# Kernel tuning notes

Hardware: AMD Instinct MI355X
Metric: run time of the kernel (lower is better)

Reference implementation:

```python
import jax, jax.numpy as jnp
import numpy as np

N = 100000      # nodes
E = 1600000     # edges (avg degree 16)
D_IN, D_H, D_OUT = 128, 128, 40
BN_EPS = 1e-5


def _gcn_norm(edge_index):
    # add self-loops, compute symmetric normalization D^-1/2 (A+I) D^-1/2
    loops = jnp.arange(N, dtype=edge_index.dtype)
    src = jnp.concatenate([edge_index[0], loops])
    dst = jnp.concatenate([edge_index[1], loops])
    deg = jax.ops.segment_sum(jnp.ones(src.shape[0], jnp.float32), dst, num_segments=N)
    dinv = jnp.where(deg > 0, jax.lax.rsqrt(deg), 0.0)
    norm = dinv[src] * dinv[dst]  # [E+N]
    return src, dst, norm


def _gcn_conv(h, W, b, src, dst, norm):
    h = h @ W                          # [N, d_out]
    msg = h[src] * norm[:, None]       # [E+N, d_out] gather + scale
    out = jax.ops.segment_sum(msg, dst, num_segments=N)
    return out + b


def _bn(h, g, beta, mean, var):
    return g * (h - mean) * jax.lax.rsqrt(var + BN_EPS) + beta


def setup_inputs() -> dict:
    key = jax.random.key(0)
    ks = jax.random.split(key, 16)
    x = jax.random.normal(ks[0], (N, D_IN), jnp.float32)
    edge_index = jax.random.randint(ks[1], (2, E), 0, N, dtype=jnp.int32)
    s_in, s_h = 1.0 / np.sqrt(D_IN), 1.0 / np.sqrt(D_H)
    W0 = jax.random.normal(ks[2], (D_IN, D_H), jnp.float32) * s_in
    b0 = jnp.zeros((D_H,), jnp.float32)
    W1 = jax.random.normal(ks[3], (D_H, D_H), jnp.float32) * s_h
    b1 = jnp.zeros((D_H,), jnp.float32)
    W2 = jax.random.normal(ks[4], (D_H, D_OUT), jnp.float32) * s_h
    b2 = jnp.zeros((D_OUT,), jnp.float32)
    g0 = jnp.ones((D_H,), jnp.float32)
    be0 = jnp.zeros((D_H,), jnp.float32)
    m0 = jax.random.normal(ks[5], (D_H,), jnp.float32) * 0.1
    v0 = jax.random.uniform(ks[6], (D_H,), jnp.float32) + 0.5
    g1 = jnp.ones((D_H,), jnp.float32)
    be1 = jnp.zeros((D_H,), jnp.float32)
    m1 = jax.random.normal(ks[7], (D_H,), jnp.float32) * 0.1
    v1 = jax.random.uniform(ks[8], (D_H,), jnp.float32) + 0.5
    return {"x": x, "edge_index": edge_index,
            "W0": W0, "b0": b0, "W1": W1, "b1": b1, "W2": W2, "b2": b2,
            "g0": g0, "be0": be0, "m0": m0, "v0": v0,
            "g1": g1, "be1": be1, "m1": m1, "v1": v1}


def reference(x, edge_index, W0, b0, W1, b1, W2, b2,
              g0, be0, m0, v0, g1, be1, m1, v1):
    src, dst, norm = _gcn_norm(edge_index)
    h = _gcn_conv(x, W0, b0, src, dst, norm)
    h = jax.nn.relu(_bn(h, g0, be0, m0, v0))   # dropout = identity in eval
    h = _gcn_conv(h, W1, b1, src, dst, norm)
    h = jax.nn.relu(_bn(h, g1, be1, m1, v1))
    h = _gcn_conv(h, W2, b2, src, dst, norm)
    return jax.nn.log_softmax(h, axis=1)
```

## Files before the change

### kernel.cpp

```cpp
#include <hip/hip_runtime.h>
#include <math.h>


#define CSHIFT 9
#define CSZ 512
#define PCHUNK 4096

typedef unsigned short u16;
typedef unsigned int u32;
typedef unsigned char u8;
typedef float f32x4 __attribute__((ext_vector_type(4)));
typedef short s16x8 __attribute__((ext_vector_type(8)));

__device__ inline float bflo(u32 u) { return __uint_as_float(u << 16); }
__device__ inline float bfhi(u32 u) { return __uint_as_float(u & 0xffff0000u); }
__device__ inline u16 f2bf(float f) {
    u32 b = __float_as_uint(f);
    b += 0x7fff + ((b >> 16) & 1);
    return (u16)(b >> 16);
}
__device__ inline u32 pack2(float lo, float hi) {
    return (u32)f2bf(lo) | ((u32)f2bf(hi) << 16);
}


__global__ __launch_bounds__(256) void k_hist1(const int* __restrict__ dst,
                                               int* __restrict__ hist1,
                                               int E, int NB) {
    __shared__ int h[256];
    int t = threadIdx.x;
    h[t] = 0;
    __syncthreads();
    for (int i = blockIdx.x * 256 * 16 + t; i < min(E, (blockIdx.x + 1) * 256 * 16);
         i += 256)
        atomicAdd(&h[dst[i] >> CSHIFT], 1);
    __syncthreads();
    if (t < NB && h[t]) atomicAdd(&hist1[t], h[t]);
}

__global__ __launch_bounds__(256) void k_scan1(const int* __restrict__ hist1,
                                               int* __restrict__ base1,
                                               int* __restrict__ cur1,
                                               int NB, int E) {
    __shared__ int sc[256];
    int t = threadIdx.x;
    int v = (t < NB) ? hist1[t] : 0;
    sc[t] = v;
    __syncthreads();
    for (int d = 1; d < 256; d <<= 1) {
        int add = (t >= d) ? sc[t - d] : 0;
        __syncthreads();
        sc[t] += add;
        __syncthreads();
    }
    if (t < NB) {
        int excl = sc[t] - v;
        base1[t] = excl;
        cur1[t] = excl;
    }
    if (t == 0) base1[NB] = E;
}

__global__ __launch_bounds__(256) void k_part1(const int* __restrict__ src,
                                               const int* __restrict__ dst,
                                               int* __restrict__ cur1,
                                               u32* __restrict__ bkt,
                                               int E, int NB) {
    __shared__ u32 stage[PCHUNK];
    __shared__ u8 sbin[PCHUNK];
    __shared__ int cnt[256];
    __shared__ int lbase[256];
    __shared__ int lcur[256];
    __shared__ int gb[256];
    int t = threadIdx.x;
    int base = blockIdx.x * PCHUNK;
    int n = min(PCHUNK, E - base);
    cnt[t] = 0;
    __syncthreads();
    for (int i = t; i < n; i += 256) atomicAdd(&cnt[dst[base + i] >> CSHIFT], 1);
    __syncthreads();
    int v = cnt[t];
    lbase[t] = v;
    __syncthreads();
    for (int d = 1; d < 256; d <<= 1) {
        int add = (t >= d) ? lbase[t - d] : 0;
        __syncthreads();
        lbase[t] += add;
        __syncthreads();
    }
    {
        int excl = lbase[t] - v;
        __syncthreads();
        lbase[t] = excl;
        lcur[t] = excl;
        if (t < NB && v) gb[t] = atomicAdd(&cur1[t], v);
    }
    __syncthreads();
    for (int i = t; i < n; i += 256) {
        int d = dst[base + i];
        int s = src[base + i];
        int bin = d >> CSHIFT;
        int p = atomicAdd(&lcur[bin], 1);
        stage[p] = ((u32)s << CSHIFT) | (u32)(d & (CSZ - 1));
        sbin[p] = (u8)bin;
    }
    __syncthreads();
    for (int k = t; k < n; k += 256) {
        int bin = sbin[k];
        bkt[gb[bin] + (k - lbase[bin])] = stage[k];
    }
}

__global__ __launch_bounds__(1024) void k_csr(const u32* __restrict__ bkt,
                                              const int* __restrict__ base1,
                                              int* __restrict__ col,
                                              int* __restrict__ row,
                                              float* __restrict__ dinv,
                                              int N, int E) {
    __shared__ int deg[CSZ];
    __shared__ int cur[CSZ];
    int b = blockIdx.x;
    int t = threadIdx.x;
    int start = base1[b];
    int end = base1[b + 1];
    if (t < CSZ) deg[t] = 0;
    __syncthreads();
    for (int i = start + t; i < end; i += 1024)
        atomicAdd(&deg[bkt[i] & (CSZ - 1)], 1);
    __syncthreads();
    int v = (t < CSZ) ? deg[t] : 0;
    if (t < CSZ) cur[t] = v;
    __syncthreads();
    for (int d = 1; d < CSZ; d <<= 1) {
        int add = (t < CSZ && t >= d) ? cur[t - d] : 0;
        __syncthreads();
        if (t < CSZ) cur[t] += add;
        __syncthreads();
    }
    if (t < CSZ) {
        int excl = cur[t] - v;
        int node = (b << CSHIFT) + t;
        if (node < N) {
            row[node] = start + excl;
            dinv[node] = rsqrtf((float)(v + 1));
        }
        cur[t] = excl;
    }
    __syncthreads();
    for (int i = start + t; i < end; i += 1024) {
        u32 e = bkt[i];
        int p = start + atomicAdd(&cur[e & (CSZ - 1)], 1);
        col[p] = (int)(e >> CSHIFT);
    }
    if (b == 0 && t == 0) row[N] = E;
}


template <int NCT, int C>
__global__ __launch_bounds__(256) void k_packW(const float* __restrict__ W,
                                               u16* __restrict__ Wpk) {
    int g = blockIdx.x * 256 + threadIdx.x;
    if (g >= NCT * 4 * 512) return;
    int j = g & 7;
    int l = (g >> 3) & 63;
    int f = g >> 9;
    int ct = f % NCT, ks = f / NCT;
    int krow = ks * 32 + ((l >> 4) << 3) + j;
    int wcol = ct * 16 + (l & 15);
    Wpk[g] = (wcol < C) ? f2bf(W[krow * C + wcol]) : (u16)0;
}


template <bool AFP32, int NCT>
__global__ __launch_bounds__(256) void k_gemmN(const void* __restrict__ Av,
                                               const u16* __restrict__ Wpk,
                                               u16* __restrict__ C,
                                               const float* __restrict__ dinv,
                                               int M, int ostride) {
    int tid = threadIdx.x;
    int wv = blockIdx.x * 4 + (tid >> 6);
    int rowbase = wv * 16;
    if (rowbase >= M) return;
    int l = tid & 63;
    int r = l & 15, hi = l >> 4;

    f32x4 acc[NCT];
#pragma unroll
    for (int ct = 0; ct < NCT; ++ct) acc[ct] = (f32x4)(0.f);

    const uint4* wp = (const uint4*)Wpk;
#pragma unroll
    for (int ks = 0; ks < 4; ++ks) {
        s16x8 afrag;
        int abase = (min(rowbase + r, M - 1)) * 128 + ks * 32 + hi * 8;
        if (AFP32) {
            const float* A = (const float*)Av;
            float4 a0 = *(const float4*)&A[abase];
            float4 a1 = *(const float4*)&A[abase + 4];
            uint4 u = make_uint4(pack2(a0.x, a0.y), pack2(a0.z, a0.w),
                                 pack2(a1.x, a1.y), pack2(a1.z, a1.w));
            afrag = *(s16x8*)&u;
        } else {
            const u16* A = (const u16*)Av;
            uint4 u = *(const uint4*)&A[abase];
            afrag = *(s16x8*)&u;
        }
#pragma unroll
        for (int ct = 0; ct < NCT; ++ct) {
            uint4 b = wp[(ks * NCT + ct) * 64 + l];
            s16x8 bfrag = *(s16x8*)&b;
            acc[ct] = __builtin_amdgcn_mfma_f32_16x16x32_bf16(afrag, bfrag, acc[ct], 0, 0, 0);
        }
    }
#pragma unroll
    for (int ct = 0; ct < NCT; ++ct) {
#pragma unroll
        for (int reg = 0; reg < 4; ++reg) {
            int orow = rowbase + 4 * hi + reg;
            int oc = ct * 16 + r;
            if (orow < M && oc < ostride)
                C[(size_t)orow * ostride + oc] = f2bf(dinv[orow] * acc[ct][reg]);
        }
    }
}


__global__ __launch_bounds__(256) void k_agg128(const u16* __restrict__ X,
                                                u16* __restrict__ Y,
                                                const int* __restrict__ row,
                                                const int* __restrict__ col,
                                                const float* __restrict__ dinv,
                                                const float* __restrict__ bias,
                                                const float* __restrict__ g,
                                                const float* __restrict__ be,
                                                const float* __restrict__ mean,
                                                const float* __restrict__ var,
                                                int n) {
    int tid = threadIdx.x;
    int wid = tid >> 6, lane = tid & 63;
    int half = lane >> 5, l5 = lane & 31;
    int node = (blockIdx.x * 4 + wid) * 2 + half;
    bool valid = node < n;
    int nc = valid ? node : (n - 1);
    const uint2* xp = (const uint2*)X;
    int s = row[nc], e = row[nc + 1];
    uint2 v = xp[(size_t)nc * 32 + l5];
    float a0 = bflo(v.x), a1 = bfhi(v.x), a2 = bflo(v.y), a3 = bfhi(v.y);
    float b0 = 0, b1 = 0, b2 = 0, b3 = 0;
    float c0 = 0, c1 = 0, c2 = 0, c3 = 0;
    float d0 = 0, d1 = 0, d2 = 0, d3 = 0;
    int j = s;
    for (; j + 8 <= e; j += 8) {
        int e0 = col[j], e1 = col[j+1], e2 = col[j+2], e3 = col[j+3];
        int e4 = col[j+4], e5 = col[j+5], e6 = col[j+6], e7 = col[j+7];
        uint2 x0 = xp[(size_t)e0 * 32 + l5];
        uint2 x1 = xp[(size_t)e1 * 32 + l5];
        uint2 x2 = xp[(size_t)e2 * 32 + l5];
        uint2 x3 = xp[(size_t)e3 * 32 + l5];
        uint2 x4 = xp[(size_t)e4 * 32 + l5];
        uint2 x5 = xp[(size_t)e5 * 32 + l5];
        uint2 x6 = xp[(size_t)e6 * 32 + l5];
        uint2 x7 = xp[(size_t)e7 * 32 + l5];
        a0 += bflo(x0.x); a1 += bfhi(x0.x); a2 += bflo(x0.y); a3 += bfhi(x0.y);
        b0 += bflo(x1.x); b1 += bfhi(x1.x); b2 += bflo(x1.y); b3 += bfhi(x1.y);
        c0 += bflo(x2.x); c1 += bfhi(x2.x); c2 += bflo(x2.y); c3 += bfhi(x2.y);
        d0 += bflo(x3.x); d1 += bfhi(x3.x); d2 += bflo(x3.y); d3 += bfhi(x3.y);
        a0 += bflo(x4.x); a1 += bfhi(x4.x); a2 += bflo(x4.y); a3 += bfhi(x4.y);
        b0 += bflo(x5.x); b1 += bfhi(x5.x); b2 += bflo(x5.y); b3 += bfhi(x5.y);
        c0 += bflo(x6.x); c1 += bfhi(x6.x); c2 += bflo(x6.y); c3 += bfhi(x6.y);
        d0 += bflo(x7.x); d1 += bfhi(x7.x); d2 += bflo(x7.y); d3 += bfhi(x7.y);
    }
    for (; j + 2 <= e; j += 2) {
        int e0 = col[j], e1 = col[j+1];
        uint2 x0 = xp[(size_t)e0 * 32 + l5];
        uint2 x1 = xp[(size_t)e1 * 32 + l5];
        a0 += bflo(x0.x); a1 += bfhi(x0.x); a2 += bflo(x0.y); a3 += bfhi(x0.y);
        b0 += bflo(x1.x); b1 += bfhi(x1.x); b2 += bflo(x1.y); b3 += bfhi(x1.y);
    }
    if (j < e) {
        uint2 x0 = xp[(size_t)col[j] * 32 + l5];
        c0 += bflo(x0.x); c1 += bfhi(x0.x); c2 += bflo(x0.y); c3 += bfhi(x0.y);
    }
    float dv = dinv[nc];
    float s0 = dv * ((a0 + b0) + (c0 + d0));
    float s1 = dv * ((a1 + b1) + (c1 + d1));
    float s2 = dv * ((a2 + b2) + (c2 + d2));
    float s3 = dv * ((a3 + b3) + (c3 + d3));
    float4 g4 = ((const float4*)g)[l5];
    float4 be4 = ((const float4*)be)[l5];
    float4 m4 = ((const float4*)mean)[l5];
    float4 v4 = ((const float4*)var)[l5];
    float4 bi4 = ((const float4*)bias)[l5];
    float sc0 = g4.x * rsqrtf(v4.x + 1e-5f);
    float sc1 = g4.y * rsqrtf(v4.y + 1e-5f);
    float sc2 = g4.z * rsqrtf(v4.z + 1e-5f);
    float sc3 = g4.w * rsqrtf(v4.w + 1e-5f);
    float y0 = fmaxf(fmaf(sc0, s0, fmaf(sc0, bi4.x - m4.x, be4.x)), 0.f);
    float y1 = fmaxf(fmaf(sc1, s1, fmaf(sc1, bi4.y - m4.y, be4.y)), 0.f);
    float y2 = fmaxf(fmaf(sc2, s2, fmaf(sc2, bi4.z - m4.z, be4.z)), 0.f);
    float y3 = fmaxf(fmaf(sc3, s3, fmaf(sc3, bi4.w - m4.w, be4.w)), 0.f);
    if (valid) {
        uint2 o;
        o.x = pack2(y0, y1);
        o.y = pack2(y2, y3);
        ((uint2*)Y)[(size_t)node * 32 + l5] = o;
    }
}

__global__ __launch_bounds__(256) void k_agg40(const u16* __restrict__ X,
                                               float* __restrict__ out,
                                               const int* __restrict__ row,
                                               const int* __restrict__ col,
                                               const float* __restrict__ dinv,
                                               const float* __restrict__ b2,
                                               int n) {
    int tid = threadIdx.x;
    int wid = tid >> 6, lane = tid & 63;
    int half = lane >> 5, l5 = lane & 31;
    int node = (blockIdx.x * 4 + wid) * 2 + half;
    bool valid = node < n;
    int nc = valid ? node : (n - 1);
    bool active = l5 < 20;
    const u32* xp = (const u32*)X;
    int s = row[nc], e = row[nc + 1];
    int li = min(l5, 19);
    float a0 = 0, a1 = 0, b0 = 0, b1 = 0, c0 = 0, c1 = 0, d0 = 0, d1 = 0;
    {
        u32 v = xp[(size_t)nc * 20 + li];
        a0 = bflo(v); a1 = bfhi(v);
    }
    int j = s;
    for (; j + 8 <= e; j += 8) {
        int e0 = col[j], e1 = col[j+1], e2 = col[j+2], e3 = col[j+3];
        int e4 = col[j+4], e5 = col[j+5], e6 = col[j+6], e7 = col[j+7];
        u32 x0 = xp[(size_t)e0 * 20 + li];
        u32 x1 = xp[(size_t)e1 * 20 + li];
        u32 x2 = xp[(size_t)e2 * 20 + li];
        u32 x3 = xp[(size_t)e3 * 20 + li];
        u32 x4 = xp[(size_t)e4 * 20 + li];
        u32 x5 = xp[(size_t)e5 * 20 + li];
        u32 x6 = xp[(size_t)e6 * 20 + li];
        u32 x7 = xp[(size_t)e7 * 20 + li];
        a0 += bflo(x0); a1 += bfhi(x0);
        b0 += bflo(x1); b1 += bfhi(x1);
        c0 += bflo(x2); c1 += bfhi(x2);
        d0 += bflo(x3); d1 += bfhi(x3);
        a0 += bflo(x4); a1 += bfhi(x4);
        b0 += bflo(x5); b1 += bfhi(x5);
        c0 += bflo(x6); c1 += bfhi(x6);
        d0 += bflo(x7); d1 += bfhi(x7);
    }
    for (; j + 2 <= e; j += 2) {
        int e0 = col[j], e1 = col[j+1];
        u32 x0 = xp[(size_t)e0 * 20 + li];
        u32 x1 = xp[(size_t)e1 * 20 + li];
        a0 += bflo(x0); a1 += bfhi(x0);
        b0 += bflo(x1); b1 += bfhi(x1);
    }
    if (j < e) {
        u32 x0 = xp[(size_t)col[j] * 20 + li];
        c0 += bflo(x0); c1 += bfhi(x0);
    }
    float dv = dinv[nc];
    float ylo = -INFINITY, yhi = -INFINITY;
    if (active) {
        float2 bb = ((const float2*)b2)[l5];
        ylo = fmaf(dv, (a0 + b0) + (c0 + d0), bb.x);
        yhi = fmaf(dv, (a1 + b1) + (c1 + d1), bb.y);
    }
    float m = fmaxf(ylo, yhi);
#pragma unroll
    for (int d = 16; d; d >>= 1) m = fmaxf(m, __shfl_xor(m, d));
    float ex = active ? (__expf(ylo - m) + __expf(yhi - m)) : 0.f;
#pragma unroll
    for (int d = 16; d; d >>= 1) ex += __shfl_xor(ex, d);
    if (valid && active) {
        float lse = m + __logf(ex);
        ((float2*)out)[(size_t)node * 20 + l5] = make_float2(ylo - lse, yhi - lse);
    }
}


extern "C" void kernel_launch(void* const* d_in, const int* in_sizes, int n_in,
                              void* d_out, int out_size, void* d_ws, size_t ws_size,
                              hipStream_t stream) {
    const float* x   = (const float*)d_in[0];
    const int*   ei  = (const int*)d_in[1];
    const float* W0  = (const float*)d_in[2];
    const float* b0  = (const float*)d_in[3];
    const float* W1  = (const float*)d_in[4];
    const float* b1  = (const float*)d_in[5];
    const float* W2  = (const float*)d_in[6];
    const float* b2  = (const float*)d_in[7];
    const float* g0  = (const float*)d_in[8];
    const float* be0 = (const float*)d_in[9];
    const float* m0  = (const float*)d_in[10];
    const float* v0  = (const float*)d_in[11];
    const float* g1  = (const float*)d_in[12];
    const float* be1 = (const float*)d_in[13];
    const float* m1  = (const float*)d_in[14];
    const float* v1  = (const float*)d_in[15];
    float* out = (float*)d_out;

    int N = in_sizes[0] / 128;
    int E = in_sizes[1] / 2;
    const int* src = ei;
    const int* dst = ei + E;

    int NB = (N + CSZ - 1) / CSZ;

    char* ws = (char*)d_ws;
    size_t off = 0;
    auto alloc = [&](size_t bytes) -> char* {
        char* p = ws + off;
        off += (bytes + 255) & ~(size_t)255;
        return p;
    };
    u16*   XsA   = (u16*)alloc((size_t)N * 128 * 2);
    u16*   XsB   = (u16*)alloc((size_t)N * 128 * 2);
    u16*   bufC  = (u16*)alloc((size_t)N * 40 * 2);
    int*   col   = (int*)alloc((size_t)E * 4 + 64);
    int*   row   = (int*)alloc((size_t)(N + 1) * 4);
    float* dinv  = (float*)alloc((size_t)N * 4);
    int*   hist1 = (int*)alloc((size_t)(NB + 1) * 4);
    int*   base1 = (int*)alloc((size_t)(NB + 1) * 4);
    int*   cur1  = (int*)alloc((size_t)(NB + 1) * 4);
    u16*   Wpk0  = (u16*)alloc(128 * 128 * 2);
    u16*   Wpk1  = (u16*)alloc(128 * 128 * 2);
    u16*   Wpk2  = (u16*)alloc(128 * 48 * 2);
    u32*   bkt   = (u32*)XsA;

    hipMemsetAsync(hist1, 0, (size_t)(NB + 1) * 4, stream);
    k_hist1<<<(E + 4095) / 4096, 256, 0, stream>>>(dst, hist1, E, NB);
    k_scan1<<<1, 256, 0, stream>>>(hist1, base1, cur1, NB, E);
    k_part1<<<(E + PCHUNK - 1) / PCHUNK, 256, 0, stream>>>(src, dst, cur1, bkt, E, NB);
    k_csr<<<NB, 1024, 0, stream>>>(bkt, base1, col, row, dinv, N, E);
    k_packW<8, 128><<<64, 256, 0, stream>>>(W0, Wpk0);
    k_packW<8, 128><<<64, 256, 0, stream>>>(W1, Wpk1);
    k_packW<3, 40><<<24, 256, 0, stream>>>(W2, Wpk2);

    int gemmGrid = ((N + 15) / 16 + 3) / 4;
    k_gemmN<true, 8><<<gemmGrid, 256, 0, stream>>>(x, Wpk0, XsA, dinv, N, 128);
    k_agg128<<<(N + 7) / 8, 256, 0, stream>>>(XsA, XsB, row, col, dinv, b0, g0, be0, m0, v0, N);
    k_gemmN<false, 8><<<gemmGrid, 256, 0, stream>>>(XsB, Wpk1, XsA, dinv, N, 128);
    k_agg128<<<(N + 7) / 8, 256, 0, stream>>>(XsA, XsB, row, col, dinv, b1, g1, be1, m1, v1, N);
    k_gemmN<false, 3><<<gemmGrid, 256, 0, stream>>>(XsB, Wpk2, bufC, dinv, N, 40);
    k_agg40<<<(N + 7) / 8, 256, 0, stream>>>(bufC, out, row, col, dinv, b2, N);
}
```

Baseline: 288.3 us.

## Store hidden features in channel-chunked layout so aggregation gathers fit cache

The 128-wide hidden features are now stored as 8 chunks of 16 channels each ([chunk][node][16]). The GEMMs write and read this tiled layout, and the aggregation kernel gives each block one chunk, so a gather only touches a 3.2 MB slice per chunk pass. The goal is better L2/MALL hit rates for the random neighbour gathers. The cost is that the column indices are re-read 8 times (now with nontemporal loads) and each gather is a smaller 8-byte access. The unroll depth also drops from 8 to 4.

```diff
diff --git a/kernel.cpp b/kernel.cpp
--- a/kernel.cpp
+++ b/kernel.cpp
@@ -11,6 +11,7 @@
 typedef unsigned char u8;
 typedef float f32x4 __attribute__((ext_vector_type(4)));
 typedef short s16x8 __attribute__((ext_vector_type(8)));
+typedef unsigned int u32x2 __attribute__((ext_vector_type(2)));
 
 __device__ inline float bflo(u32 u) { return __uint_as_float(u << 16); }
 __device__ inline float bfhi(u32 u) { return __uint_as_float(u & 0xffff0000u); }
@@ -171,7 +172,7 @@
 }
 
 
-template <bool AFP32, int NCT>
+template <bool AFP32, bool ATILED, int NCT, bool OTILED>
 __global__ __launch_bounds__(256) void k_gemmN(const void* __restrict__ Av,
                                                const u16* __restrict__ Wpk,
                                                u16* __restrict__ C,
@@ -183,6 +184,7 @@
     if (rowbase >= M) return;
     int l = tid & 63;
     int r = l & 15, hi = l >> 4;
+    int arow = min(rowbase + r, M - 1);
 
     f32x4 acc[NCT];
 #pragma unroll
@@ -192,17 +194,23 @@
 #pragma unroll
     for (int ks = 0; ks < 4; ++ks) {
         s16x8 afrag;
-        int abase = (min(rowbase + r, M - 1)) * 128 + ks * 32 + hi * 8;
         if (AFP32) {
             const float* A = (const float*)Av;
+            int abase = arow * 128 + ks * 32 + hi * 8;
             float4 a0 = *(const float4*)&A[abase];
             float4 a1 = *(const float4*)&A[abase + 4];
             uint4 u = make_uint4(pack2(a0.x, a0.y), pack2(a0.z, a0.w),
                                  pack2(a1.x, a1.y), pack2(a1.z, a1.w));
             afrag = *(s16x8*)&u;
+        } else if (ATILED) {
+            const u16* A = (const u16*)Av;
+            int k0 = ks * 32 + hi * 8;
+            int ch = k0 >> 4, off = k0 & 15;
+            uint4 u = *(const uint4*)&A[((size_t)ch * M + arow) * 16 + off];
+            afrag = *(s16x8*)&u;
         } else {
             const u16* A = (const u16*)Av;
-            uint4 u = *(const uint4*)&A[abase];
+            uint4 u = *(const uint4*)&A[(size_t)arow * 128 + ks * 32 + hi * 8];
             afrag = *(s16x8*)&u;
         }
 #pragma unroll
@@ -218,79 +226,77 @@
         for (int reg = 0; reg < 4; ++reg) {
             int orow = rowbase + 4 * hi + reg;
             int oc = ct * 16 + r;
-            if (orow < M && oc < ostride)
-                C[(size_t)orow * ostride + oc] = f2bf(dinv[orow] * acc[ct][reg]);
+            if (orow < M && oc < ostride) {
+                u16 val = f2bf(dinv[orow] * acc[ct][reg]);
+                if (OTILED)
+                    C[((size_t)ct * M + orow) * 16 + r] = val;
+                else
+                    C[(size_t)orow * ostride + oc] = val;
+            }
         }
     }
 }
 
 
-__global__ __launch_bounds__(256) void k_agg128(const u16* __restrict__ X,
-                                                u16* __restrict__ Y,
-                                                const int* __restrict__ row,
-                                                const int* __restrict__ col,
-                                                const float* __restrict__ dinv,
-                                                const float* __restrict__ bias,
-                                                const float* __restrict__ g,
-                                                const float* __restrict__ be,
-                                                const float* __restrict__ mean,
-                                                const float* __restrict__ var,
-                                                int n) {
+__global__ __launch_bounds__(256) void k_agg128t(const u16* __restrict__ X,
+                                                 u16* __restrict__ Y,
+                                                 const int* __restrict__ row,
+                                                 const int* __restrict__ col,
+                                                 const float* __restrict__ dinv,
+                                                 const float* __restrict__ bias,
+                                                 const float* __restrict__ g,
+                                                 const float* __restrict__ be,
+                                                 const float* __restrict__ mean,
+                                                 const float* __restrict__ var,
+                                                 int n) {
     int tid = threadIdx.x;
-    int wid = tid >> 6, lane = tid & 63;
-    int half = lane >> 5, l5 = lane & 31;
-    int node = (blockIdx.x * 4 + wid) * 2 + half;
+    int ch = blockIdx.x & 7;
+    int nblk = blockIdx.x >> 3;
+    int wid = tid >> 6, l = tid & 63;
+    int gi = l >> 2, li = l & 3;
+    int node = nblk * 64 + wid * 16 + gi;
     bool valid = node < n;
     int nc = valid ? node : (n - 1);
-    const uint2* xp = (const uint2*)X;
+    const u16* Xc = X + (size_t)ch * n * 16;
     int s = row[nc], e = row[nc + 1];
-    uint2 v = xp[(size_t)nc * 32 + l5];
+    int fo = li * 4;
+
+    uint2 v = *(const uint2*)&Xc[(size_t)nc * 16 + fo];
     float a0 = bflo(v.x), a1 = bfhi(v.x), a2 = bflo(v.y), a3 = bfhi(v.y);
     float b0 = 0, b1 = 0, b2 = 0, b3 = 0;
     float c0 = 0, c1 = 0, c2 = 0, c3 = 0;
     float d0 = 0, d1 = 0, d2 = 0, d3 = 0;
     int j = s;
-    for (; j + 8 <= e; j += 8) {
-        int e0 = col[j], e1 = col[j+1], e2 = col[j+2], e3 = col[j+3];
-        int e4 = col[j+4], e5 = col[j+5], e6 = col[j+6], e7 = col[j+7];
-        uint2 x0 = xp[(size_t)e0 * 32 + l5];
-        uint2 x1 = xp[(size_t)e1 * 32 + l5];
-        uint2 x2 = xp[(size_t)e2 * 32 + l5];
-        uint2 x3 = xp[(size_t)e3 * 32 + l5];
-        uint2 x4 = xp[(size_t)e4 * 32 + l5];
-        uint2 x5 = xp[(size_t)e5 * 32 + l5];
-        uint2 x6 = xp[(size_t)e6 * 32 + l5];
-        uint2 x7 = xp[(size_t)e7 * 32 + l5];
+    for (; j + 4 <= e; j += 4) {
+        int e0 = __builtin_nontemporal_load(col + j);
+        int e1 = __builtin_nontemporal_load(col + j + 1);
+        int e2 = __builtin_nontemporal_load(col + j + 2);
+        int e3 = __builtin_nontemporal_load(col + j + 3);
+        uint2 x0 = *(const uint2*)&Xc[(size_t)e0 * 16 + fo];
+        uint2 x1 = *(const uint2*)&Xc[(size_t)e1 * 16 + fo];
+        uint2 x2 = *(const uint2*)&Xc[(size_t)e2 * 16 + fo];
+        uint2 x3 = *(const uint2*)&Xc[(size_t)e3 * 16 + fo];
         a0 += bflo(x0.x); a1 += bfhi(x0.x); a2 += bflo(x0.y); a3 += bfhi(x0.y);
         b0 += bflo(x1.x); b1 += bfhi(x1.x); b2 += bflo(x1.y); b3 += bfhi(x1.y);
         c0 += bflo(x2.x); c1 += bfhi(x2.x); c2 += bflo(x2.y); c3 += bfhi(x2.y);
         d0 += bflo(x3.x); d1 += bfhi(x3.x); d2 += bflo(x3.y); d3 += bfhi(x3.y);
-        a0 += bflo(x4.x); a1 += bfhi(x4.x); a2 += bflo(x4.y); a3 += bfhi(x4.y);
-        b0 += bflo(x5.x); b1 += bfhi(x5.x); b2 += bflo(x5.y); b3 += bfhi(x5.y);
-        c0 += bflo(x6.x); c1 += bfhi(x6.x); c2 += bflo(x6.y); c3 += bfhi(x6.y);
-        d0 += bflo(x7.x); d1 += bfhi(x7.x); d2 += bflo(x7.y); d3 += bfhi(x7.y);
-    }
-    for (; j + 2 <= e; j += 2) {
-        int e0 = col[j], e1 = col[j+1];
-        uint2 x0 = xp[(size_t)e0 * 32 + l5];
-        uint2 x1 = xp[(size_t)e1 * 32 + l5];
+    }
+    for (; j < e; ++j) {
+        int e0 = __builtin_nontemporal_load(col + j);
+        uint2 x0 = *(const uint2*)&Xc[(size_t)e0 * 16 + fo];
         a0 += bflo(x0.x); a1 += bfhi(x0.x); a2 += bflo(x0.y); a3 += bfhi(x0.y);
-        b0 += bflo(x1.x); b1 += bfhi(x1.x); b2 += bflo(x1.y); b3 += bfhi(x1.y);
-    }
-    if (j < e) {
-        uint2 x0 = xp[(size_t)col[j] * 32 + l5];
-        c0 += bflo(x0.x); c1 += bfhi(x0.x); c2 += bflo(x0.y); c3 += bfhi(x0.y);
     }
     float dv = dinv[nc];
     float s0 = dv * ((a0 + b0) + (c0 + d0));
     float s1 = dv * ((a1 + b1) + (c1 + d1));
     float s2 = dv * ((a2 + b2) + (c2 + d2));
     float s3 = dv * ((a3 + b3) + (c3 + d3));
-    float4 g4 = ((const float4*)g)[l5];
-    float4 be4 = ((const float4*)be)[l5];
-    float4 m4 = ((const float4*)mean)[l5];
-    float4 v4 = ((const float4*)var)[l5];
-    float4 bi4 = ((const float4*)bias)[l5];
+    int pidx = ch * 4 + li;
+    float4 g4 = ((const float4*)g)[pidx];
+    float4 be4 = ((const float4*)be)[pidx];
+    float4 m4 = ((const float4*)mean)[pidx];
+    float4 v4 = ((const float4*)var)[pidx];
+    float4 bi4 = ((const float4*)bias)[pidx];
     float sc0 = g4.x * rsqrtf(v4.x + 1e-5f);
     float sc1 = g4.y * rsqrtf(v4.y + 1e-5f);
     float sc2 = g4.z * rsqrtf(v4.z + 1e-5f);
@@ -300,12 +306,13 @@
     float y2 = fmaxf(fmaf(sc2, s2, fmaf(sc2, bi4.z - m4.z, be4.z)), 0.f);
     float y3 = fmaxf(fmaf(sc3, s3, fmaf(sc3, bi4.w - m4.w, be4.w)), 0.f);
     if (valid) {
-        uint2 o;
+        u32x2 o;
         o.x = pack2(y0, y1);
         o.y = pack2(y2, y3);
-        ((uint2*)Y)[(size_t)node * 32 + l5] = o;
-    }
-}
+        __builtin_nontemporal_store(o, (u32x2*)&Y[((size_t)ch * n + node) * 16 + fo]);
+    }
+}
+
 
 __global__ __launch_bounds__(256) void k_agg40(const u16* __restrict__ X,
                                                float* __restrict__ out,
@@ -430,7 +437,8 @@
     u16*   Wpk2  = (u16*)alloc(128 * 48 * 2);
     u32*   bkt   = (u32*)XsA;
 
-    hipMemsetAsync(hist1, 0, (size_t)(NB + 1) * 4, stream);
+    hipError_t _e = hipMemsetAsync(hist1, 0, (size_t)(NB + 1) * 4, stream);
+    (void)_e;
     k_hist1<<<(E + 4095) / 4096, 256, 0, stream>>>(dst, hist1, E, NB);
     k_scan1<<<1, 256, 0, stream>>>(hist1, base1, cur1, NB, E);
     k_part1<<<(E + PCHUNK - 1) / PCHUNK, 256, 0, stream>>>(src, dst, cur1, bkt, E, NB);
@@ -439,11 +447,12 @@
     k_packW<8, 128><<<64, 256, 0, stream>>>(W1, Wpk1);
     k_packW<3, 40><<<24, 256, 0, stream>>>(W2, Wpk2);
 
-    int gemmGrid = ((N + 15) / 16 + 3) / 4;
-    k_gemmN<true, 8><<<gemmGrid, 256, 0, stream>>>(x, Wpk0, XsA, dinv, N, 128);
-    k_agg128<<<(N + 7) / 8, 256, 0, stream>>>(XsA, XsB, row, col, dinv, b0, g0, be0, m0, v0, N);
-    k_gemmN<false, 8><<<gemmGrid, 256, 0, stream>>>(XsB, Wpk1, XsA, dinv, N, 128);
-    k_agg128<<<(N + 7) / 8, 256, 0, stream>>>(XsA, XsB, row, col, dinv, b1, g1, be1, m1, v1, N);
-    k_gemmN<false, 3><<<gemmGrid, 256, 0, stream>>>(XsB, Wpk2, bufC, dinv, N, 40);
+    int gemmGrid = (N + 63) / 64;
+    int aggGrid = 8 * ((N + 63) / 64);
+    k_gemmN<true, false, 8, true><<<gemmGrid, 256, 0, stream>>>(x, Wpk0, XsA, dinv, N, 128);
+    k_agg128t<<<aggGrid, 256, 0, stream>>>(XsA, XsB, row, col, dinv, b0, g0, be0, m0, v0, N);
+    k_gemmN<false, true, 8, true><<<gemmGrid, 256, 0, stream>>>(XsB, Wpk1, XsA, dinv, N, 128);
+    k_agg128t<<<aggGrid, 256, 0, stream>>>(XsA, XsB, row, col, dinv, b1, g1, be1, m1, v1, N);
+    k_gemmN<false, true, 3, false><<<gemmGrid, 256, 0, stream>>>(XsB, Wpk2, bufC, dinv, N, 40);
     k_agg40<<<(N + 7) / 8, 256, 0, stream>>>(bufC, out, row, col, dinv, b2, N);
 }
```

Measured after the change: 443.5 us. 1.54x slower.
